# Performance work log

Measured on AMD Instinct MI355X. Metric: run time of the kernel, lower is better.

The kernel has to match this reference:

```python
import jax, jax.numpy as jnp
import numpy as np

K_CONST = 1.0  # margin constant K from __init__


def setup_inputs() -> dict:
    key = jax.random.key(0)
    k1, k2, k3 = jax.random.split(key, 3)
    m, n, d = 2048, 100000, 128
    return {
        "X_tilde": jax.random.normal(k1, (m, d), dtype=jnp.float32),
        "X": jax.random.normal(k2, (n, d), dtype=jnp.float32),
        "w": jax.random.normal(k3, (n, 1), dtype=jnp.float32),
        "k": 10,
    }


def reference(X_tilde, X, w, k):
    # w_prime = sqrt((max(w) - w) / K), appended as extra coordinate for the
    # augmented exact L2 search (queries padded with 0 in that coordinate).
    w_prime2 = (jnp.max(w) - w)[:, 0] / K_CONST  # (n,) == w_prime**2
    # squared L2 in augmented space: ||q||^2 + ||x||^2 + w_prime^2 - 2 q.x
    q2 = jnp.sum(X_tilde * X_tilde, axis=1, keepdims=True)           # (m,1)
    x2 = jnp.sum(X * X, axis=1) + w_prime2                            # (n,)
    d2 = q2 + x2[None, :] - 2.0 * (X_tilde @ X.T)                     # (m,n)
    _, idx = jax.lax.top_k(-d2, k)                                    # (m,k) nearest
    # gather neighbors and recompute actual (non-augmented) L2 distance
    nb = X[idx]                                                       # (m,k,d)
    diff = nb - X_tilde[:, None, :]
    dist = jnp.sqrt(jnp.sum(diff * diff, axis=2))                     # (m,k)
    act = w[idx, 0] - K_CONST * dist                                  # (m,k)
    # argmax + gather == max over the k neighbors
    return jnp.max(act, axis=1)                                       # (m,)
```

## Files before the change

### kernel.cpp

```cpp
#include <hip/hip_runtime.h>
#include <math.h>

typedef __attribute__((ext_vector_type(8))) short short8;
typedef __attribute__((ext_vector_type(16))) float f32x16;

#define D      128
#define NSEG   128
#define SEGC   800
#define NT     25
#define TPP    5
#define NPART  5
#define TILE_C 32
#define KTOP   10
#define CAP    128
#define DELTA  3.0f
#define NPAD   (NSEG * SEGC + TILE_C)
#define ROWU   144
#define TUNITS (TILE_C * 18)
#define BUFU   (TUNITS * 8)
#define MQ     2048
#define WQCAP  (NSEG * 8 * NPART)

__device__ __forceinline__ int lds_unit(int u) {
    int r = u / 18, kb = u % 18;
    return r * 18 + (kb ^ ((r >> 2) & 1));
}

__device__ __forceinline__ ushort f2bf(float f) {
    uint u = __float_as_uint(f);
    uint r = (u + 0x7FFFu + ((u >> 16) & 1u)) >> 16;
    return (ushort)r;
}

__device__ __forceinline__ uint packx2(float x2w) {
    ushort h = f2bf(x2w);
    float hf = __uint_as_float(((uint)h) << 16);
    ushort lo = f2bf(x2w - hf);
    return (uint)h | ((uint)lo << 16);
}

__device__ __forceinline__ void insert10(float s, float v, float ls[KTOP], float lw[KTOP]) {
    ls[9] = s; lw[9] = v;
#pragma unroll
    for (int p = 9; p > 0; --p) {
        bool sw = ls[p] < ls[p - 1];
        float ts = sw ? ls[p - 1] : ls[p];
        float tl = sw ? ls[p]     : ls[p - 1];
        float tv = sw ? lw[p - 1] : lw[p];
        float tu = sw ? lw[p]     : lw[p - 1];
        ls[p] = ts; ls[p - 1] = tl;
        lw[p] = tv; lw[p - 1] = tu;
    }
}

__device__ __forceinline__ void insert10s(float s, float ms[KTOP]) {
    ms[9] = s;
#pragma unroll
    for (int p = 9; p > 0; --p) {
        float a = fminf(ms[p - 1], ms[p]);
        float b = fmaxf(ms[p - 1], ms[p]);
        ms[p - 1] = a; ms[p] = b;
    }
}

__global__ void prep_kernel(const float* __restrict__ Xt, const float* __restrict__ X,
                            const float* __restrict__ w,
                            ushort* __restrict__ Xbp, ushort* __restrict__ Xtb,
                            float* __restrict__ x2wf, float* __restrict__ q2f,
                            int* __restrict__ cnt, int* __restrict__ wq_n,
                            int n, int m, int nblocksA) {
    if (blockIdx.x == 0 && threadIdx.x == 0) wq_n[0] = 0;
    int wave = threadIdx.x >> 6, lane = threadIdx.x & 63;
    if ((int)blockIdx.x < nblocksA) {
        int row = blockIdx.x * 4 + wave;
        if (row >= NPAD) return;
        ushort* rowp = Xbp + (size_t)row * ROWU;
        if (row < n) {
            float2 v = ((const float2*)X)[(size_t)row * 64 + lane];
            ((ushort2*)rowp)[lane] = make_ushort2(f2bf(v.x), f2bf(v.y));
            float s = v.x * v.x + v.y * v.y;
#pragma unroll
            for (int o = 32; o; o >>= 1) s += __shfl_xor(s, o, 64);
            float x2w = s - w[row];
            if (lane == 0) x2wf[row] = x2w;
            if (lane < 8) ((uint*)rowp)[64 + lane] = (lane == 0) ? packx2(x2w) : 0u;
        } else {
            ((ushort2*)rowp)[lane] = make_ushort2(0, 0);
            if (lane < 8) ((uint*)rowp)[64 + lane] = (lane == 0) ? packx2(1e30f) : 0u;
        }
    } else {
        int qb = blockIdx.x - nblocksA;
        int row = qb * 4 + wave;
        int tid = qb * 256 + threadIdx.x;
        if (tid < m) cnt[tid] = 0;
        if (row >= m) return;
        float2 v = ((const float2*)Xt)[(size_t)row * 64 + lane];
        ((ushort2*)Xtb)[(size_t)row * 64 + lane] = make_ushort2(f2bf(v.x), f2bf(v.y));
        float s = v.x * v.x + v.y * v.y;
#pragma unroll
        for (int o = 32; o; o >>= 1) s += __shfl_xor(s, o, 64);
        if (lane == 0) q2f[row] = s;
    }
}

__device__ __forceinline__ void emit_cand(int q, int c, int* cnt, int* buf) {
    int pos = atomicAdd(&cnt[q], 1);
    if (pos < CAP) buf[q * CAP + pos] = c;
}

__global__ __launch_bounds__(256, 4) void nd_pass1(
        const ushort* __restrict__ Xbp, const ushort* __restrict__ Xtb,
        float* __restrict__ minbuf, int m) {
    __shared__ __align__(16) ushort As[2 * BUFU];

    const int t = threadIdx.x;
    const int l = t & 63, wv = t >> 6;
    const int half = l >> 5;
    const int seg = blockIdx.x;
    const int qbase = blockIdx.y * 256 + wv * 64;
    const int q0 = qbase + (l & 31);
    const int tile0 = seg * NT;
    const int halfx = half ^ ((l >> 2) & 1);

    short8 Bf[8][2];
#pragma unroll
    for (int s = 0; s < 8; ++s)
#pragma unroll
        for (int qs = 0; qs < 2; ++qs)
            Bf[s][qs] = *(const short8*)(Xtb + (size_t)(q0 + qs * 32) * D + s * 16 + half * 8);
    short8 B8 = (short8)(short)0;
    if (l < 32) { B8[0] = (short)0xBF00; B8[1] = (short)0xBF00; }

    float mx0 = -INFINITY, mx1 = -INFINITY;

    const int u0 = t, u1 = 256 + t, u2 = 512 + (t & 63);
    const int L0 = lds_unit(u0) * 8, L1 = lds_unit(u1) * 8, L2 = lds_unit(u2) * 8;
    const uint4* Xg = (const uint4*)Xbp;

    uint4 r0 = Xg[(size_t)tile0 * TUNITS + u0];
    uint4 r1 = Xg[(size_t)tile0 * TUNITS + u1];
    uint4 r2 = make_uint4(0, 0, 0, 0);
    if (t < 64) r2 = Xg[(size_t)tile0 * TUNITS + u2];

    for (int t2 = 0; t2 < NT; ++t2) {
        ushort* Lb = &As[(t2 & 1) * BUFU];
        *(uint4*)&Lb[L0] = r0;
        *(uint4*)&Lb[L1] = r1;
        if (t < 64) *(uint4*)&Lb[L2] = r2;
        __syncthreads();

        const size_t gb = (size_t)(tile0 + t2 + 1) * TUNITS;
        r0 = Xg[gb + u0];
        r1 = Xg[gb + u1];
        if (t < 64) r2 = Xg[gb + u2];

        f32x16 acc0 = (f32x16)0.f, acc1 = (f32x16)0.f;
#pragma unroll
        for (int ks = 0; ks < 9; ++ks) {
            const int kb = (ks < 8) ? (ks * 2 + halfx) : (16 + halfx);
            short8 a = *(const short8*)&Lb[((l & 31) * 18 + kb) * 8];
            short8 b0 = (ks < 8) ? Bf[ks][0] : B8;
            short8 b1 = (ks < 8) ? Bf[ks][1] : B8;
            acc0 = __builtin_amdgcn_mfma_f32_32x32x16_bf16(a, b0, acc0, 0, 0, 0);
            acc1 = __builtin_amdgcn_mfma_f32_32x32x16_bf16(a, b1, acc1, 0, 0, 0);
        }

        float h0 = -INFINITY, h1 = -INFINITY;
#pragma unroll
        for (int r = 0; r < 16; ++r) { h0 = fmaxf(h0, acc0[r]); h1 = fmaxf(h1, acc1[r]); }
        mx0 = fmaxf(mx0, h0);
        mx1 = fmaxf(mx1, h1);
    }

    size_t rowi = (size_t)(seg * 2 + half) * m;
    minbuf[rowi + q0]      = -2.f * mx0;
    minbuf[rowi + q0 + 32] = -2.f * mx1;
}

__global__ void tau_kernel(const float* __restrict__ minbuf, float* __restrict__ tau, int m) {
    __shared__ float sh[64 * 40];
    const int qi = threadIdx.x & 63, part = threadIdx.x >> 6;
    const int q = blockIdx.x * 64 + qi;
    float ms[KTOP];
#pragma unroll
    for (int e = 0; e < KTOP; ++e) ms[e] = INFINITY;
#pragma unroll 4
    for (int i = 0; i < 64; ++i) {
        float v = minbuf[(size_t)(part * 64 + i) * m + q];
        if (v < ms[9]) insert10s(v, ms);
    }
#pragma unroll
    for (int e = 0; e < KTOP; ++e) sh[qi * 40 + part * 10 + e] = ms[e];
    __syncthreads();
    if (threadIdx.x < 64) {
        const int qq = blockIdx.x * 64 + threadIdx.x;
        float fs[KTOP];
#pragma unroll
        for (int e = 0; e < KTOP; ++e) fs[e] = INFINITY;
        for (int x = 0; x < 40; ++x) {
            float v = sh[threadIdx.x * 40 + x];
            if (v < fs[9]) insert10s(v, fs);
        }
        tau[qq] = fs[9] + DELTA;
    }
}

__global__ void list_build(const float* __restrict__ minbuf, const float* __restrict__ tau,
                           int* __restrict__ qlist, int* __restrict__ wq,
                           int* __restrict__ wq_n, int m) {
    __shared__ int lq[MQ];
    __shared__ int lcnt;
    const int s = blockIdx.x, tid = threadIdx.x;
    if (tid == 0) lcnt = 0;
    __syncthreads();
    const float* r0 = minbuf + (size_t)(2 * s) * m;
    const float* r1 = minbuf + (size_t)(2 * s + 1) * m;
    for (int q = tid; q < m; q += 256) {
        float v = fminf(r0[q], r1[q]);
        if (v <= tau[q]) { int p = atomicAdd(&lcnt, 1); lq[p] = q; }
    }
    __syncthreads();
    const int c = lcnt;
    const int padded = (c + 255) & ~255;
    for (int i = c + tid; i < padded; i += 256) lq[i] = -1;
    __syncthreads();
    for (int i = tid; i < padded; i += 256) qlist[(size_t)s * MQ + i] = lq[i];
    if (tid == 0 && c > 0) {
        const int nqc = padded >> 8;
        int base = atomicAdd(wq_n, nqc * NPART);
        for (int qc = 0; qc < nqc; ++qc)
            for (int p = 0; p < NPART; ++p)
                wq[base++] = (s << 6) | (qc << 3) | p;
    }
}

__global__ __launch_bounds__(256, 4) void nd_pass2(
        const ushort* __restrict__ Xbp, const ushort* __restrict__ Xtb,
        const float* __restrict__ tau,
        int* __restrict__ cnt, int* __restrict__ buf,
        const int* __restrict__ qlist, const int* __restrict__ wq,
        const int* __restrict__ wq_n, int m) {
    __shared__ __align__(16) ushort As[2 * BUFU];

    const int t = threadIdx.x;
    const int l = t & 63, wv = t >> 6;
    const int half = l >> 5;
    const int halfx = half ^ ((l >> 2) & 1);
    const int u0 = t, u1 = 256 + t, u2 = 512 + (t & 63);
    const int L0 = lds_unit(u0) * 8, L1 = lds_unit(u1) * 8, L2 = lds_unit(u2) * 8;
    const uint4* Xg = (const uint4*)Xbp;
    const int T = wq_n[0];

    for (int w = blockIdx.x; w < T; w += gridDim.x) {
        const int it = wq[w];
        const int s = it >> 6, qc = (it >> 3) & 7, part = it & 7;
        const int t0 = s * NT + part * TPP;
        const int lbase = s * MQ + qc * 256 + wv * 64 + (l & 31);
        const int qi0 = qlist[lbase], qi1 = qlist[lbase + 32];
        const int q0e = qi0 < 0 ? 0 : qi0, q1e = qi1 < 0 ? 0 : qi1;

        short8 Bf[8][2];
#pragma unroll
        for (int sk = 0; sk < 8; ++sk) {
            Bf[sk][0] = *(const short8*)(Xtb + (size_t)q0e * D + sk * 16 + half * 8);
            Bf[sk][1] = *(const short8*)(Xtb + (size_t)q1e * D + sk * 16 + half * 8);
        }
        short8 B8 = (short8)(short)0;
        if (l < 32) { B8[0] = (short)0xBF00; B8[1] = (short)0xBF00; }
        const float tp0 = (qi0 < 0) ? INFINITY : (-0.5f * tau[qi0]);
        const float tp1 = (qi1 < 0) ? INFINITY : (-0.5f * tau[qi1]);

        uint4 r0 = Xg[(size_t)t0 * TUNITS + u0];
        uint4 r1 = Xg[(size_t)t0 * TUNITS + u1];
        uint4 r2 = make_uint4(0, 0, 0, 0);
        if (t < 64) r2 = Xg[(size_t)t0 * TUNITS + u2];

        for (int t2 = t0; t2 < t0 + TPP; ++t2) {
            ushort* Lb = &As[(t2 & 1) * BUFU];
            *(uint4*)&Lb[L0] = r0;
            *(uint4*)&Lb[L1] = r1;
            if (t < 64) *(uint4*)&Lb[L2] = r2;
            __syncthreads();

            const size_t gb = (size_t)(t2 + 1) * TUNITS;
            r0 = Xg[gb + u0];
            r1 = Xg[gb + u1];
            if (t < 64) r2 = Xg[gb + u2];

            f32x16 acc0 = (f32x16)0.f, acc1 = (f32x16)0.f;
#pragma unroll
            for (int ks = 0; ks < 9; ++ks) {
                const int kb = (ks < 8) ? (ks * 2 + halfx) : (16 + halfx);
                short8 a = *(const short8*)&Lb[((l & 31) * 18 + kb) * 8];
                short8 b0 = (ks < 8) ? Bf[ks][0] : B8;
                short8 b1 = (ks < 8) ? Bf[ks][1] : B8;
                acc0 = __builtin_amdgcn_mfma_f32_32x32x16_bf16(a, b0, acc0, 0, 0, 0);
                acc1 = __builtin_amdgcn_mfma_f32_32x32x16_bf16(a, b1, acc1, 0, 0, 0);
            }

            float h0 = -INFINITY, h1 = -INFINITY;
#pragma unroll
            for (int r = 0; r < 16; ++r) { h0 = fmaxf(h0, acc0[r]); h1 = fmaxf(h1, acc1[r]); }
            const int base = t2 * TILE_C;
            if (__any(h0 >= tp0)) {
#pragma unroll
                for (int r = 0; r < 16; ++r)
                    if (acc0[r] >= tp0) emit_cand(qi0, base + (r & 3) + 8 * (r >> 2) + 4 * half, cnt, buf);
            }
            if (__any(h1 >= tp1)) {
#pragma unroll
                for (int r = 0; r < 16; ++r)
                    if (acc1[r] >= tp1) emit_cand(qi1, base + (r & 3) + 8 * (r >> 2) + 4 * half, cnt, buf);
            }
        }
        __syncthreads();
    }
}

__global__ void rescore_kernel(const float* __restrict__ Xtf, const float* __restrict__ Xf,
                               const float* __restrict__ w, const float* __restrict__ x2wf,
                               const float* __restrict__ q2f, const int* __restrict__ cnt,
                               const int* __restrict__ buf, float* __restrict__ out, int m) {
    __shared__ float sS[CAP], sW[CAP];
    const int q = blockIdx.x, l = threadIdx.x;
    const int c = min(cnt[q], CAP);
    const bool v0 = l < c, v1 = l + 64 < c;
    const int j0 = v0 ? buf[q * CAP + l] : 0;
    const int j1 = v1 ? buf[q * CAP + l + 64] : 0;
    const float4* Q4 = (const float4*)Xtf + (size_t)q * 32;
    const float4* A4 = (const float4*)Xf + (size_t)j0 * 32;
    const float4* B4 = (const float4*)Xf + (size_t)j1 * 32;
    float acc0 = 0.f, acc1 = 0.f;
#pragma unroll 8
    for (int d = 0; d < 32; ++d) {
        float4 qv = Q4[d];
        float4 a = A4[d], b = B4[d];
        acc0 = fmaf(qv.x, a.x, fmaf(qv.y, a.y, fmaf(qv.z, a.z, fmaf(qv.w, a.w, acc0))));
        acc1 = fmaf(qv.x, b.x, fmaf(qv.y, b.y, fmaf(qv.z, b.z, fmaf(qv.w, b.w, acc1))));
    }
    sS[l]      = v0 ? (x2wf[j0] - 2.f * acc0) : INFINITY;
    sW[l]      = v0 ? w[j0] : 0.f;
    sS[l + 64] = v1 ? (x2wf[j1] - 2.f * acc1) : INFINITY;
    sW[l + 64] = v1 ? w[j1] : 0.f;
    __syncthreads();
    if (l == 0) {
        float ls[KTOP], lw[KTOP];
#pragma unroll
        for (int e = 0; e < KTOP; ++e) { ls[e] = INFINITY; lw[e] = 0.f; }
        for (int i = 0; i < c; ++i)
            if (sS[i] < ls[9]) insert10(sS[i], sW[i], ls, lw);
        float q2v = q2f[q];
        float mxv = -INFINITY;
#pragma unroll
        for (int e = 0; e < KTOP; ++e) {
            if (ls[e] < 1e30f) {
                float d2 = fmaxf(q2v + ls[e] + lw[e], 0.f);
                mxv = fmaxf(mxv, lw[e] - sqrtf(d2));
            }
        }
        out[q] = mxv;
    }
}

extern "C" void kernel_launch(void* const* d_in, const int* in_sizes, int n_in,
                              void* d_out, int out_size, void* d_ws, size_t ws_size,
                              hipStream_t stream) {
    const float* Xt = (const float*)d_in[0];
    const float* X  = (const float*)d_in[1];
    const float* w  = (const float*)d_in[2];
    const int m = in_sizes[0] / D;
    const int n = in_sizes[1] / D;

    auto align256 = [](size_t x) { return (x + 255) & ~(size_t)255; };
    char* p = (char*)d_ws;
    ushort* Xbp  = (ushort*)p;  p += align256((size_t)NPAD * ROWU * 2);
    ushort* Xtb  = (ushort*)p;  p += align256((size_t)m * D * 2);
    float*  x2wf = (float*)p;   p += align256((size_t)n * 4);
    float*  q2f  = (float*)p;   p += align256((size_t)m * 4);
    float*  minb = (float*)p;   p += align256((size_t)2 * NSEG * m * 4);
    float*  tau  = (float*)p;   p += align256((size_t)m * 4);
    int*    cnt  = (int*)p;     p += align256((size_t)m * 4);
    int*    buf  = (int*)p;     p += align256((size_t)m * CAP * 4);
    int*    qlist= (int*)p;     p += align256((size_t)NSEG * MQ * 4);
    int*    wq   = (int*)p;     p += align256((size_t)WQCAP * 4);
    int*    wq_n = (int*)p;     p += align256((size_t)256);

    const int nblocksA = (NPAD + 3) / 4;
    const int nblocksB = (m + 3) / 4;
    prep_kernel<<<nblocksA + nblocksB, 256, 0, stream>>>(Xt, X, w, Xbp, Xtb, x2wf, q2f,
                                                         cnt, wq_n, n, m, nblocksA);

    dim3 grid1(NSEG, m / 256);
    nd_pass1<<<grid1, 256, 0, stream>>>(Xbp, Xtb, minb, m);
    tau_kernel<<<m / 64, 256, 0, stream>>>(minb, tau, m);
    list_build<<<NSEG, 256, 0, stream>>>(minb, tau, qlist, wq, wq_n, m);
    nd_pass2<<<1024, 256, 0, stream>>>(Xbp, Xtb, tau, cnt, buf, qlist, wq, wq_n, m);
    rescore_kernel<<<m, 64, 0, stream>>>(Xt, X, w, x2wf, q2f, cnt, buf, (float*)d_out, m);
}
```

Baseline: 251.6 us.

## Stage pass1 tiles with direct global-to-LDS loads in a 4-deep ring

```diff
diff --git a/kernel.cpp b/kernel.cpp
--- a/kernel.cpp
+++ b/kernel.cpp
@@ -14,9 +14,10 @@
 #define KTOP   10
 #define CAP    128
 #define DELTA  3.0f
-#define NPAD   (NSEG * SEGC + TILE_C)
+#define NPAD   (NSEG * SEGC + 3 * TILE_C)
 #define ROWU   144
 #define TUNITS (TILE_C * 18)
+#define TBYTES (TUNITS * 16)
 #define BUFU   (TUNITS * 8)
 #define MQ     2048
 #define WQCAP  (NSEG * 8 * NPART)
@@ -24,6 +25,17 @@
 __device__ __forceinline__ int lds_unit(int u) {
     int r = u / 18, kb = u % 18;
     return r * 18 + (kb ^ ((r >> 2) & 1));
+}
+
+__device__ __forceinline__ void gl_lds16(const void* g, void* lds) {
+    __builtin_amdgcn_global_load_lds(
+        (const __attribute__((address_space(1))) unsigned int*)g,
+        (__attribute__((address_space(3))) unsigned int*)lds, 16, 0, 0);
+}
+__device__ __forceinline__ void gl_lds4(const void* g, void* lds) {
+    __builtin_amdgcn_global_load_lds(
+        (const __attribute__((address_space(1))) unsigned int*)g,
+        (__attribute__((address_space(3))) unsigned int*)lds, 4, 0, 0);
 }
 
 __device__ __forceinline__ ushort f2bf(float f) {
@@ -111,7 +123,7 @@
 __global__ __launch_bounds__(256, 4) void nd_pass1(
         const ushort* __restrict__ Xbp, const ushort* __restrict__ Xtb,
         float* __restrict__ minbuf, int m) {
-    __shared__ __align__(16) ushort As[2 * BUFU];
+    __shared__ __align__(16) ushort As[4 * BUFU];
 
     const int t = threadIdx.x;
     const int l = t & 63, wv = t >> 6;
@@ -133,27 +145,32 @@
 
     float mx0 = -INFINITY, mx1 = -INFINITY;
 
-    const int u0 = t, u1 = 256 + t, u2 = 512 + (t & 63);
-    const int L0 = lds_unit(u0) * 8, L1 = lds_unit(u1) * 8, L2 = lds_unit(u2) * 8;
-    const uint4* Xg = (const uint4*)Xbp;
-
-    uint4 r0 = Xg[(size_t)tile0 * TUNITS + u0];
-    uint4 r1 = Xg[(size_t)tile0 * TUNITS + u1];
-    uint4 r2 = make_uint4(0, 0, 0, 0);
-    if (t < 64) r2 = Xg[(size_t)tile0 * TUNITS + u2];
+    const int off0 = lds_unit(wv * 144 + l) * 16;
+    const int off1 = lds_unit(wv * 144 + 64 + l) * 16;
+    const int off2 = lds_unit(wv * 144 + 128 + (l >> 2)) * 16 + (l & 3) * 4;
+    const int db = wv * 2304;
+    const char* Xc = (const char*)Xbp;
+    char* Ac = (char*)As;
+
+    auto stage = [&](int T, int b) {
+        const char* s = Xc + (size_t)T * TBYTES;
+        char* d = Ac + b * TBYTES + db;
+        gl_lds16(s + off0, d);
+        gl_lds16(s + off1, d + 1024);
+        gl_lds4 (s + off2, d + 2048);
+    };
+
+    stage(tile0 + 0, 0);
+    stage(tile0 + 1, 1);
+    stage(tile0 + 2, 2);
 
     for (int t2 = 0; t2 < NT; ++t2) {
-        ushort* Lb = &As[(t2 & 1) * BUFU];
-        *(uint4*)&Lb[L0] = r0;
-        *(uint4*)&Lb[L1] = r1;
-        if (t < 64) *(uint4*)&Lb[L2] = r2;
-        __syncthreads();
-
-        const size_t gb = (size_t)(tile0 + t2 + 1) * TUNITS;
-        r0 = Xg[gb + u0];
-        r1 = Xg[gb + u1];
-        if (t < 64) r2 = Xg[gb + u2];
-
+        asm volatile("s_waitcnt vmcnt(6)" ::: "memory");
+        __builtin_amdgcn_sched_barrier(0);
+        __builtin_amdgcn_s_barrier();
+        stage(tile0 + t2 + 3, (t2 + 3) & 3);
+
+        const ushort* Lb = &As[(t2 & 3) * BUFU];
         f32x16 acc0 = (f32x16)0.f, acc1 = (f32x16)0.f;
 #pragma unroll
         for (int ks = 0; ks < 9; ++ks) {
```

Measured after the change: 244.9 us. -2.7%, faster.
